# Kernel tuning notes

Hardware: AMD Instinct MI355X
Metric: run time of the kernel (lower is better)

Reference implementation:

```python
import jax, jax.numpy as jnp
import numpy as np

B, C_IN, C_OUT, H, W, K = 8, 32, 32, 96, 96, 5


def setup_inputs() -> dict:
    key = jax.random.key(0)
    k1, k2 = jax.random.split(key)
    f = jax.random.normal(k1, (B, C_IN, H, W), dtype=jnp.float32)
    # xavier_uniform-style init for the structuring element h
    fan_in = C_IN * K * K
    fan_out = C_OUT * K * K
    bound = float(np.sqrt(6.0 / (fan_in + fan_out)))
    h = jax.random.uniform(k2, (C_OUT, C_IN, K, K), dtype=jnp.float32,
                           minval=-bound, maxval=bound)
    return {"f": f, "h": h}


def reference(f, h):
    """Morphological max-plus dilation with 'same' padding.

    out[b,o,y,x] = max_{c,i,j} f[b,c,y+i-p, x+j-p] + h[o,c,i,j]
    """
    b, c, hh, ww = f.shape
    o, _, k, _ = h.shape
    p = k // 2
    neg = -jnp.finfo(f.dtype).max / 2
    fp = jnp.pad(f, ((0, 0), (0, 0), (p, p), (p, p)), constant_values=neg)
    out = jnp.full((b, o, hh, ww), neg, dtype=f.dtype)
    for i in range(k):          # fixed small kernel loop (k*k = 25 taps)
        for j in range(k):
            sl = fp[:, :, i:i + hh, j:j + ww]              # (B, C, H, W)
            w_ij = h[:, :, i, j]                            # (O, C)
            # max-plus over input channels: (B,1,C,H,W) + (O,C,1,1)
            cand = jnp.max(sl[:, None] + w_ij[None, :, :, None, None], axis=2)
            out = jnp.maximum(out, cand)
    return out
```

## Files before the change

### kernel.cpp

```cpp
#include <hip/hip_runtime.h>


#define B_ 8
#define C_ 32
#define O_ 32
#define H_ 96
#define W_ 96
#define K_ 5
#define KK_ (K_ * K_)
#define NCP_ (C_ / 2)

#define TX_ 24
#define RT_ 4
#define CS_ 4
#define TY_ (RT_ * CS_)
#define NT_ (TX_ * TY_)
#define XR_ 4
#define OB_ 4
#define CPG_ (NCP_ / CS_)

#define PH_ 100
#define PW_ 104
#define PLSZ_ (PH_ * PW_)
#define FPAD_BYTES ((size_t)B_ * NCP_ * PLSZ_ * 4)

#define NEGF (-30000.0f)

typedef _Float16 h2 __attribute__((ext_vector_type(2)));

static __device__ __forceinline__ h2 h2b(unsigned u) {
    return __builtin_bit_cast(h2, u);
}
static __device__ __forceinline__ unsigned bh2(h2 v) {
    return __builtin_bit_cast(unsigned, v);
}

static __device__ __forceinline__ void pk_fmamax(h2& acc, h2 fv, h2 hv, h2 one) {
    h2 t;
    asm("v_pk_fma_f16 %0, %1, %2, %3" : "=v"(t) : "v"(fv), "v"(one), "v"(hv));
    asm("v_pk_max_f16 %0, %1, %2" : "=v"(acc) : "v"(acc), "v"(t));
}

__global__ __launch_bounds__(256)
void prepad_kernel(const float* __restrict__ f, unsigned* __restrict__ fpad) {
    const int idx = blockIdx.x * 256 + threadIdx.x;
    const int cp = blockIdx.y;
    const int b  = blockIdx.z;
    if (idx >= PLSZ_) return;
    const int row = idx / PW_;
    const int col = idx - row * PW_;
    const int y = row - 2;
    const int x = col - 2;
    float v0 = NEGF, v1 = NEGF;
    if ((unsigned)y < H_ && (unsigned)x < W_) {
        v0 = f[((size_t)(b * C_ + 2 * cp)     * H_ + y) * W_ + x];
        v1 = f[((size_t)(b * C_ + 2 * cp + 1) * H_ + y) * W_ + x];
    }
    h2 d; d.x = (_Float16)v0; d.y = (_Float16)v1;
    fpad[(size_t)(b * NCP_ + cp) * PLSZ_ + idx] = bh2(d);
}

template <bool PADDED>
__global__ __launch_bounds__(NT_)
void dilate_main(const unsigned* __restrict__ fpad,
                 const float* __restrict__ f,
                 const float* __restrict__ h, float* __restrict__ out) {
    const int tx  = threadIdx.x;
    const int ty  = threadIdx.y;
    const int tid = ty * TX_ + tx;
    const int ry  = ty & (RT_ - 1);
    const int g   = ty >> 2;

    const int ytile = blockIdx.x;
    const int og    = blockIdx.y;
    const int b     = blockIdx.z;
    const int y0 = ytile * RT_;
    const int o0 = og * OB_;
    const int x0 = XR_ * tx;
    const int yb = y0 + ry;

    __shared__ unsigned hs2[NCP_][104];
    __shared__ unsigned short comb[CS_ - 1][OB_ * XR_][RT_ * TX_];

    for (int idx = tid; idx < NCP_ * KK_ * OB_; idx += NT_) {
        int cp = idx / (KK_ * OB_);
        int rr = idx - cp * (KK_ * OB_);
        int ij = rr / OB_;
        int o  = rr - ij * OB_;
        float a0 = h[((size_t)(o0 + o) * C_ + 2 * cp)     * KK_ + ij];
        float a1 = h[((size_t)(o0 + o) * C_ + 2 * cp + 1) * KK_ + ij];
        h2 p; p.x = (_Float16)a0; p.y = (_Float16)a1;
        hs2[cp][ij * OB_ + o] = bh2(p);
    }
    __syncthreads();

    h2 acc[OB_][XR_];
    h2 one;
    {
        h2 neg; neg.x = (_Float16)NEGF; neg.y = (_Float16)NEGF;
        one.x = (_Float16)1.0f; one.y = (_Float16)1.0f;
#pragma unroll
        for (int o = 0; o < OB_; ++o)
#pragma unroll
            for (int xx = 0; xx < XR_; ++xx) acc[o][xx] = neg;
    }

    const int cp0 = g * CPG_;
    for (int cpi = 0; cpi < CPG_; ++cpi) {
        const int cp = cp0 + cpi;

        h2 win[K_][8];
        if (PADDED) {
            const unsigned* p =
                fpad + (size_t)(b * NCP_ + cp) * PLSZ_ + yb * PW_ + x0;
#pragma unroll
            for (int i = 0; i < K_; ++i) {
                const uint4* q = (const uint4*)(p + i * PW_);
                uint4 w0 = q[0];
                uint4 w1 = q[1];
                win[i][0] = h2b(w0.x); win[i][1] = h2b(w0.y);
                win[i][2] = h2b(w0.z); win[i][3] = h2b(w0.w);
                win[i][4] = h2b(w1.x); win[i][5] = h2b(w1.y);
                win[i][6] = h2b(w1.z); win[i][7] = h2b(w1.w);
            }
        } else {
            const float* fc0 = f + (size_t)(b * C_ + 2 * cp) * (H_ * W_);
            const float* fc1 = f + (size_t)(b * C_ + 2 * cp + 1) * (H_ * W_);
#pragma unroll
            for (int i = 0; i < K_; ++i) {
#pragma unroll
                for (int q = 0; q < 8; ++q) {
                    int yy = yb + i - 2;
                    int xc = x0 - 2 + q;
                    bool ok = ((unsigned)yy < H_) && ((unsigned)xc < W_);
                    float v0 = ok ? fc0[(size_t)yy * W_ + xc] : NEGF;
                    float v1 = ok ? fc1[(size_t)yy * W_ + xc] : NEGF;
                    h2 d; d.x = (_Float16)v0; d.y = (_Float16)v1;
                    win[i][q] = d;
                }
            }
        }

#pragma unroll
        for (int i = 0; i < K_; ++i) {
#pragma unroll
            for (int j = 0; j < K_; ++j) {
                uint4 hq = *(const uint4*)&hs2[cp][(i * K_ + j) * OB_];
                h2 h0 = h2b(hq.x), h1 = h2b(hq.y);
                h2 h02 = h2b(hq.z), h3 = h2b(hq.w);
#pragma unroll
                for (int xx = 0; xx < XR_; ++xx) {
                    h2 fv = win[i][xx + j];
                    pk_fmamax(acc[0][xx], fv, h0, one);
                    pk_fmamax(acc[1][xx], fv, h1, one);
                    pk_fmamax(acc[2][xx], fv, h02, one);
                    pk_fmamax(acc[3][xx], fv, h3, one);
                }
            }
        }
    }

    unsigned short red[OB_][XR_];
#pragma unroll
    for (int o = 0; o < OB_; ++o)
#pragma unroll
        for (int xx = 0; xx < XR_; ++xx) {
            _Float16 a = acc[o][xx].x;
            _Float16 b2 = acc[o][xx].y;
            _Float16 m = (a > b2) ? a : b2;
            red[o][xx] = __builtin_bit_cast(unsigned short, m);
        }

    const int t96 = ry * TX_ + tx;
    if (g > 0) {
#pragma unroll
        for (int o = 0; o < OB_; ++o)
#pragma unroll
            for (int xx = 0; xx < XR_; ++xx)
                comb[g - 1][o * XR_ + xx][t96] = red[o][xx];
    }
    __syncthreads();
    if (g == 0) {
        const int y = yb;
#pragma unroll
        for (int o = 0; o < OB_; ++o) {
            float r[XR_];
#pragma unroll
            for (int xx = 0; xx < XR_; ++xx) {
                const int row = o * XR_ + xx;
                _Float16 m = __builtin_bit_cast(_Float16, red[o][xx]);
                _Float16 v0 = __builtin_bit_cast(_Float16, comb[0][row][t96]);
                _Float16 v1 = __builtin_bit_cast(_Float16, comb[1][row][t96]);
                _Float16 v2 = __builtin_bit_cast(_Float16, comb[2][row][t96]);
                m = (v0 > m) ? v0 : m;
                m = (v1 > m) ? v1 : m;
                m = (v2 > m) ? v2 : m;
                r[xx] = (float)m;
            }
            float4 v = make_float4(r[0], r[1], r[2], r[3]);
            *(float4*)&out[(((size_t)b * O_ + (o0 + o)) * H_ + y) * W_ + x0] = v;
        }
    }
}

extern "C" void kernel_launch(void* const* d_in, const int* in_sizes, int n_in,
                              void* d_out, int out_size, void* d_ws, size_t ws_size,
                              hipStream_t stream) {
    const float* f = (const float*)d_in[0];
    const float* h = (const float*)d_in[1];
    float* out = (float*)d_out;

    dim3 mgrid(H_ / RT_, O_ / OB_, B_);
    dim3 mblock(TX_, TY_);

    if (ws_size >= FPAD_BYTES) {
        unsigned* fpad = (unsigned*)d_ws;
        dim3 pgrid((PLSZ_ + 255) / 256, NCP_, B_);
        hipLaunchKernelGGL(prepad_kernel, pgrid, dim3(256), 0, stream, f, fpad);
        hipLaunchKernelGGL((dilate_main<true>), mgrid, mblock, 0, stream,
                           fpad, f, h, out);
    } else {
        hipLaunchKernelGGL((dilate_main<false>), mgrid, mblock, 0, stream,
                           (const unsigned*)nullptr, f, h, out);
    }
}
```

Measured before the change: 146.8 us.

## Load structuring-element weights into SGPRs via scalar loads and use pk_add

Adds a separate kernel that packs h into a per-output-group fp16 layout in the workspace. The main kernel then reads the weights with wave-uniform s_load_dwordx8 into scalar registers and uses v_pk_add_f16 with an SGPR operand, replacing the LDS weight reads and the pk_fma-by-one. The block shape moves from 4 rows x 4 channel splits to 8 rows x 2 splits, which shrinks the cross-split reduction. The costs are an extra launch, heavy SGPR pressure, explicit waitcnt stalls inside the loop, and a slow naive fallback when the workspace is too small.

```diff
diff --git a/kernel.cpp b/kernel.cpp
--- a/kernel.cpp
+++ b/kernel.cpp
@@ -11,8 +11,8 @@
 #define NCP_ (C_ / 2)
 
 #define TX_ 24
-#define RT_ 4
-#define CS_ 4
+#define RT_ 8
+#define CS_ 2
 #define TY_ (RT_ * CS_)
 #define NT_ (TX_ * TY_)
 #define XR_ 4
@@ -24,9 +24,14 @@
 #define PLSZ_ (PH_ * PW_)
 #define FPAD_BYTES ((size_t)B_ * NCP_ * PLSZ_ * 4)
 
+#define HBLK_ 128
+#define HPACK_DW (8 * NCP_ * HBLK_)
+
 #define NEGF (-30000.0f)
 
 typedef _Float16 h2 __attribute__((ext_vector_type(2)));
+typedef int sv8 __attribute__((ext_vector_type(8)));
+typedef int sv4 __attribute__((ext_vector_type(4)));
 
 static __device__ __forceinline__ h2 h2b(unsigned u) {
     return __builtin_bit_cast(h2, u);
@@ -35,10 +40,25 @@
     return __builtin_bit_cast(unsigned, v);
 }
 
-static __device__ __forceinline__ void pk_fmamax(h2& acc, h2 fv, h2 hv, h2 one) {
+static __device__ __forceinline__ void pk_addmax_s(h2& acc, h2 fv, int hs) {
     h2 t;
-    asm("v_pk_fma_f16 %0, %1, %2, %3" : "=v"(t) : "v"(fv), "v"(one), "v"(hv));
+    asm("v_pk_add_f16 %0, %1, %2" : "=v"(t) : "v"(fv), "s"(hs));
     asm("v_pk_max_f16 %0, %1, %2" : "=v"(acc) : "v"(acc), "v"(t));
+}
+
+static __device__ __forceinline__ int hgetA(sv8 a0, sv8 a1, sv8 a2, sv8 a3,
+                                            sv8 a4, sv8 a5, int n) {
+    if (n < 8)  return a0[n];
+    if (n < 16) return a1[n - 8];
+    if (n < 24) return a2[n - 16];
+    if (n < 32) return a3[n - 24];
+    if (n < 40) return a4[n - 32];
+    return a5[n - 40];
+}
+static __device__ __forceinline__ int hgetB(sv8 a0, sv8 a1, sv8 a2, sv8 a3,
+                                            sv8 a4, sv8 a5, sv4 b, int n) {
+    if (n < 48) return hgetA(a0, a1, a2, a3, a4, a5, n);
+    return b[n - 48];
 }
 
 __global__ __launch_bounds__(256)
@@ -60,16 +80,31 @@
     fpad[(size_t)(b * NCP_ + cp) * PLSZ_ + idx] = bh2(d);
 }
 
-template <bool PADDED>
+__global__ __launch_bounds__(256)
+void hpack_kernel(const float* __restrict__ h, unsigned* __restrict__ hpack) {
+    const int idx = blockIdx.x * 256 + threadIdx.x;
+    if (idx >= 8 * NCP_ * KK_ * OB_) return;
+    const int og = idx / (NCP_ * KK_ * OB_);
+    int r  = idx - og * (NCP_ * KK_ * OB_);
+    const int cp = r / (KK_ * OB_);
+    r -= cp * (KK_ * OB_);
+    const int ij = r / OB_;
+    const int o  = r - ij * OB_;
+    float a0 = h[((size_t)(og * OB_ + o) * C_ + 2 * cp)     * KK_ + ij];
+    float a1 = h[((size_t)(og * OB_ + o) * C_ + 2 * cp + 1) * KK_ + ij];
+    h2 p; p.x = (_Float16)a0; p.y = (_Float16)a1;
+    hpack[(size_t)(og * NCP_ + cp) * HBLK_ + ij * OB_ + o] = bh2(p);
+}
+
 __global__ __launch_bounds__(NT_)
 void dilate_main(const unsigned* __restrict__ fpad,
-                 const float* __restrict__ f,
-                 const float* __restrict__ h, float* __restrict__ out) {
+                 const unsigned* __restrict__ hpack,
+                 float* __restrict__ out) {
     const int tx  = threadIdx.x;
     const int ty  = threadIdx.y;
-    const int tid = ty * TX_ + tx;
     const int ry  = ty & (RT_ - 1);
-    const int g   = ty >> 2;
+    const int g   = ty >> 3;
+    const int gu  = __builtin_amdgcn_readfirstlane(g);
 
     const int ytile = blockIdx.x;
     const int og    = blockIdx.y;
@@ -79,40 +114,24 @@
     const int x0 = XR_ * tx;
     const int yb = y0 + ry;
 
-    __shared__ unsigned hs2[NCP_][104];
-    __shared__ unsigned short comb[CS_ - 1][OB_ * XR_][RT_ * TX_];
-
-    for (int idx = tid; idx < NCP_ * KK_ * OB_; idx += NT_) {
-        int cp = idx / (KK_ * OB_);
-        int rr = idx - cp * (KK_ * OB_);
-        int ij = rr / OB_;
-        int o  = rr - ij * OB_;
-        float a0 = h[((size_t)(o0 + o) * C_ + 2 * cp)     * KK_ + ij];
-        float a1 = h[((size_t)(o0 + o) * C_ + 2 * cp + 1) * KK_ + ij];
-        h2 p; p.x = (_Float16)a0; p.y = (_Float16)a1;
-        hs2[cp][ij * OB_ + o] = bh2(p);
-    }
-    __syncthreads();
+    __shared__ unsigned short comb[OB_ * XR_][RT_ * TX_];
 
     h2 acc[OB_][XR_];
-    h2 one;
     {
         h2 neg; neg.x = (_Float16)NEGF; neg.y = (_Float16)NEGF;
-        one.x = (_Float16)1.0f; one.y = (_Float16)1.0f;
 #pragma unroll
         for (int o = 0; o < OB_; ++o)
 #pragma unroll
             for (int xx = 0; xx < XR_; ++xx) acc[o][xx] = neg;
     }
 
-    const int cp0 = g * CPG_;
+    const int cp0v = g * CPG_;
+    const int cp0s = gu * CPG_;
     for (int cpi = 0; cpi < CPG_; ++cpi) {
-        const int cp = cp0 + cpi;
-
         h2 win[K_][8];
-        if (PADDED) {
-            const unsigned* p =
-                fpad + (size_t)(b * NCP_ + cp) * PLSZ_ + yb * PW_ + x0;
+        {
+            const unsigned* p = fpad +
+                (size_t)(b * NCP_ + cp0v + cpi) * PLSZ_ + yb * PW_ + x0;
 #pragma unroll
             for (int i = 0; i < K_; ++i) {
                 const uint4* q = (const uint4*)(p + i * PW_);
@@ -123,39 +142,71 @@
                 win[i][4] = h2b(w1.x); win[i][5] = h2b(w1.y);
                 win[i][6] = h2b(w1.z); win[i][7] = h2b(w1.w);
             }
-        } else {
-            const float* fc0 = f + (size_t)(b * C_ + 2 * cp) * (H_ * W_);
-            const float* fc1 = f + (size_t)(b * C_ + 2 * cp + 1) * (H_ * W_);
-#pragma unroll
-            for (int i = 0; i < K_; ++i) {
-#pragma unroll
-                for (int q = 0; q < 8; ++q) {
-                    int yy = yb + i - 2;
-                    int xc = x0 - 2 + q;
-                    bool ok = ((unsigned)yy < H_) && ((unsigned)xc < W_);
-                    float v0 = ok ? fc0[(size_t)yy * W_ + xc] : NEGF;
-                    float v1 = ok ? fc1[(size_t)yy * W_ + xc] : NEGF;
-                    h2 d; d.x = (_Float16)v0; d.y = (_Float16)v1;
-                    win[i][q] = d;
-                }
-            }
-        }
-
-#pragma unroll
-        for (int i = 0; i < K_; ++i) {
-#pragma unroll
-            for (int j = 0; j < K_; ++j) {
-                uint4 hq = *(const uint4*)&hs2[cp][(i * K_ + j) * OB_];
-                h2 h0 = h2b(hq.x), h1 = h2b(hq.y);
-                h2 h02 = h2b(hq.z), h3 = h2b(hq.w);
-#pragma unroll
-                for (int xx = 0; xx < XR_; ++xx) {
-                    h2 fv = win[i][xx + j];
-                    pk_fmamax(acc[0][xx], fv, h0, one);
-                    pk_fmamax(acc[1][xx], fv, h1, one);
-                    pk_fmamax(acc[2][xx], fv, h02, one);
-                    pk_fmamax(acc[3][xx], fv, h3, one);
-                }
+        }
+
+        const unsigned* hp =
+            hpack + (size_t)(og * NCP_ + cp0s + cpi) * HBLK_;
+
+        sv8 a0, a1, a2, a3, a4, a5;
+        asm volatile(
+            "s_load_dwordx8 %0, %6, 0x0\n\t"
+            "s_load_dwordx8 %1, %6, 0x20\n\t"
+            "s_load_dwordx8 %2, %6, 0x40\n\t"
+            "s_load_dwordx8 %3, %6, 0x60\n\t"
+            "s_load_dwordx8 %4, %6, 0x80\n\t"
+            "s_load_dwordx8 %5, %6, 0xa0\n\t"
+            "s_waitcnt lgkmcnt(0)"
+            : "=s"(a0), "=s"(a1), "=s"(a2), "=s"(a3), "=s"(a4), "=s"(a5)
+            : "s"(hp));
+
+#pragma unroll
+        for (int ij = 0; ij < 12; ++ij) {
+            const int i = ij / K_, j = ij % K_;
+            const int n = ij * 4;
+            int h0 = hgetA(a0, a1, a2, a3, a4, a5, n);
+            int h1 = hgetA(a0, a1, a2, a3, a4, a5, n + 1);
+            int h2v = hgetA(a0, a1, a2, a3, a4, a5, n + 2);
+            int h3 = hgetA(a0, a1, a2, a3, a4, a5, n + 3);
+#pragma unroll
+            for (int xx = 0; xx < XR_; ++xx) {
+                h2 fv = win[i][xx + j];
+                pk_addmax_s(acc[0][xx], fv, h0);
+                pk_addmax_s(acc[1][xx], fv, h1);
+                pk_addmax_s(acc[2][xx], fv, h2v);
+                pk_addmax_s(acc[3][xx], fv, h3);
+            }
+        }
+
+        sv8 b0, b1, b2, b3, b4, b5;
+        sv4 bt;
+        asm volatile(
+            "s_load_dwordx8 %0, %7, 0xc0\n\t"
+            "s_load_dwordx8 %1, %7, 0xe0\n\t"
+            "s_load_dwordx8 %2, %7, 0x100\n\t"
+            "s_load_dwordx8 %3, %7, 0x120\n\t"
+            "s_load_dwordx8 %4, %7, 0x140\n\t"
+            "s_load_dwordx8 %5, %7, 0x160\n\t"
+            "s_load_dwordx4 %6, %7, 0x180\n\t"
+            "s_waitcnt lgkmcnt(0)"
+            : "=s"(b0), "=s"(b1), "=s"(b2), "=s"(b3), "=s"(b4), "=s"(b5),
+              "=s"(bt)
+            : "s"(hp));
+
+#pragma unroll
+        for (int ij = 12; ij < KK_; ++ij) {
+            const int i = ij / K_, j = ij % K_;
+            const int n = ij * 4 - 48;
+            int h0 = hgetB(b0, b1, b2, b3, b4, b5, bt, n);
+            int h1 = hgetB(b0, b1, b2, b3, b4, b5, bt, n + 1);
+            int h2v = hgetB(b0, b1, b2, b3, b4, b5, bt, n + 2);
+            int h3 = hgetB(b0, b1, b2, b3, b4, b5, bt, n + 3);
+#pragma unroll
+            for (int xx = 0; xx < XR_; ++xx) {
+                h2 fv = win[i][xx + j];
+                pk_addmax_s(acc[0][xx], fv, h0);
+                pk_addmax_s(acc[1][xx], fv, h1);
+                pk_addmax_s(acc[2][xx], fv, h2v);
+                pk_addmax_s(acc[3][xx], fv, h3);
             }
         }
     }
@@ -171,13 +222,13 @@
             red[o][xx] = __builtin_bit_cast(unsigned short, m);
         }
 
-    const int t96 = ry * TX_ + tx;
-    if (g > 0) {
+    const int t192 = ry * TX_ + tx;
+    if (g == 1) {
 #pragma unroll
         for (int o = 0; o < OB_; ++o)
 #pragma unroll
             for (int xx = 0; xx < XR_; ++xx)
-                comb[g - 1][o * XR_ + xx][t96] = red[o][xx];
+                comb[o * XR_ + xx][t192] = red[o][xx];
     }
     __syncthreads();
     if (g == 0) {
@@ -187,20 +238,39 @@
             float r[XR_];
 #pragma unroll
             for (int xx = 0; xx < XR_; ++xx) {
-                const int row = o * XR_ + xx;
-                _Float16 m = __builtin_bit_cast(_Float16, red[o][xx]);
-                _Float16 v0 = __builtin_bit_cast(_Float16, comb[0][row][t96]);
-                _Float16 v1 = __builtin_bit_cast(_Float16, comb[1][row][t96]);
-                _Float16 v2 = __builtin_bit_cast(_Float16, comb[2][row][t96]);
+                _Float16 m  = __builtin_bit_cast(_Float16, red[o][xx]);
+                _Float16 v0 = __builtin_bit_cast(_Float16,
+                                                 comb[o * XR_ + xx][t192]);
                 m = (v0 > m) ? v0 : m;
-                m = (v1 > m) ? v1 : m;
-                m = (v2 > m) ? v2 : m;
                 r[xx] = (float)m;
             }
             float4 v = make_float4(r[0], r[1], r[2], r[3]);
             *(float4*)&out[(((size_t)b * O_ + (o0 + o)) * H_ + y) * W_ + x0] = v;
         }
     }
+}
+
+__global__ __launch_bounds__(256)
+void dilate_naive(const float* __restrict__ f, const float* __restrict__ h,
+                  float* __restrict__ out) {
+    const int idx = blockIdx.x * 256 + threadIdx.x;
+    if (idx >= B_ * O_ * H_ * W_) return;
+    const int x = idx % W_;
+    const int y = (idx / W_) % H_;
+    const int o = (idx / (W_ * H_)) % O_;
+    const int b = idx / (W_ * H_ * O_);
+    float m = -3.0e38f;
+    for (int c = 0; c < C_; ++c)
+        for (int i = 0; i < K_; ++i)
+            for (int j = 0; j < K_; ++j) {
+                int yy = y + i - 2, xc = x + j - 2;
+                if ((unsigned)yy < H_ && (unsigned)xc < W_) {
+                    float v = f[((size_t)(b * C_ + c) * H_ + yy) * W_ + xc] +
+                              h[((size_t)o * C_ + c) * KK_ + i * K_ + j];
+                    m = fmaxf(m, v);
+                }
+            }
+    out[idx] = m;
 }
 
 extern "C" void kernel_launch(void* const* d_in, const int* in_sizes, int n_in,
@@ -210,17 +280,22 @@
     const float* h = (const float*)d_in[1];
     float* out = (float*)d_out;
 
-    dim3 mgrid(H_ / RT_, O_ / OB_, B_);
-    dim3 mblock(TX_, TY_);
-
-    if (ws_size >= FPAD_BYTES) {
-        unsigned* fpad = (unsigned*)d_ws;
+    const size_t need = FPAD_BYTES + (size_t)HPACK_DW * 4;
+    if (ws_size >= need) {
+        unsigned* fpad  = (unsigned*)d_ws;
+        unsigned* hpack = (unsigned*)((char*)d_ws + FPAD_BYTES);
         dim3 pgrid((PLSZ_ + 255) / 256, NCP_, B_);
         hipLaunchKernelGGL(prepad_kernel, pgrid, dim3(256), 0, stream, f, fpad);
-        hipLaunchKernelGGL((dilate_main<true>), mgrid, mblock, 0, stream,
-                           fpad, f, h, out);
+        hipLaunchKernelGGL(hpack_kernel,
+                           dim3((8 * NCP_ * KK_ * OB_ + 255) / 256), dim3(256),
+                           0, stream, h, hpack);
+        dim3 mgrid(H_ / RT_, O_ / OB_, B_);
+        dim3 mblock(TX_, TY_);
+        hipLaunchKernelGGL(dilate_main, mgrid, mblock, 0, stream,
+                           fpad, hpack, out);
     } else {
-        hipLaunchKernelGGL((dilate_main<false>), mgrid, mblock, 0, stream,
-                           (const unsigned*)nullptr, f, h, out);
-    }
-}
+        hipLaunchKernelGGL(dilate_naive,
+                           dim3((B_ * O_ * H_ * W_ + 255) / 256), dim3(256),
+                           0, stream, f, h, out);
+    }
+}
```

Result: faster. 139.9 us (-4.7%).
